# Kernel tuning notes

Measured on AMD Instinct MI355X. Metric: run time of the kernel, lower is better.

The kernel has to match this reference:

```python
import jax, jax.numpy as jnp
import numpy as np

B, HGRID, WGRID = 4, 32, 32
L = 1 + HGRID * WGRID          # cls token + spatial tokens
INPUT_DIM = 512
HEAD_DIM = 512
N_HEAD = 8
QKV_DIM = HEAD_DIM * N_HEAD    # 4096


def pos_embed_2d(h, w, C, dtype):
    """Standard 2D sinusoidal positional embedding, shape (h*w, C)."""
    d = C // 4
    omega = 1.0 / (10000.0 ** (jnp.arange(d, dtype=jnp.float32) / d))
    ey = jnp.arange(h, dtype=jnp.float32)[:, None] * omega      # (h, d)
    ex = jnp.arange(w, dtype=jnp.float32)[:, None] * omega      # (w, d)
    emb_y = jnp.concatenate([jnp.sin(ey), jnp.cos(ey)], -1)     # (h, 2d)
    emb_x = jnp.concatenate([jnp.sin(ex), jnp.cos(ex)], -1)     # (w, 2d)
    emb = jnp.concatenate([
        jnp.broadcast_to(emb_y[:, None, :], (h, w, 2 * d)),
        jnp.broadcast_to(emb_x[None, :, :], (h, w, 2 * d)),
    ], -1)                                                       # (h, w, C)
    return emb.reshape(h * w, C).astype(dtype)


def setup_inputs() -> dict:
    key = jax.random.key(0)
    ks = jax.random.split(key, 16)
    s = 0.02
    inp = {
        "x": jax.random.normal(ks[0], (B, L, INPUT_DIM), dtype=jnp.float32),
        # Q/K/V linear: weight (out, in) as in torch Linear, bias zeros (per _init_bias)
        "Wq": jax.random.normal(ks[1], (QKV_DIM, INPUT_DIM), jnp.float32) * s,
        "bq": jnp.zeros((QKV_DIM,), jnp.float32),
        "Wk": jax.random.normal(ks[2], (QKV_DIM, INPUT_DIM), jnp.float32) * s,
        "bk": jnp.zeros((QKV_DIM,), jnp.float32),
        "Wv": jax.random.normal(ks[3], (QKV_DIM, INPUT_DIM), jnp.float32) * s,
        "bv": jnp.zeros((QKV_DIM,), jnp.float32),
        # 1x1 conv poolers: weight (out_ch, in_ch) = (HEAD_DIM, HEAD_DIM)
        "Wpq": jax.random.normal(ks[4], (HEAD_DIM, HEAD_DIM), jnp.float32) * s,
        "bpq": jax.random.normal(ks[5], (HEAD_DIM,), jnp.float32) * s,
        "Wpk": jax.random.normal(ks[6], (HEAD_DIM, HEAD_DIM), jnp.float32) * s,
        "bpk": jax.random.normal(ks[7], (HEAD_DIM,), jnp.float32) * s,
        "Wpv": jax.random.normal(ks[8], (HEAD_DIM, HEAD_DIM), jnp.float32) * s,
        "bpv": jax.random.normal(ks[9], (HEAD_DIM,), jnp.float32) * s,
        # dispatcher linear: (INPUT_DIM, QKV_DIM)
        "Wd": jax.random.normal(ks[10], (INPUT_DIM, QKV_DIM), jnp.float32) * s,
        "bd": jax.random.normal(ks[11], (INPUT_DIM,), jnp.float32) * s,
        "h": HGRID,
        "w": WGRID,
    }
    return inp


def _pool(t, Wp, bp):
    """AttentionPooler with kernel=1/stride=1: pointwise conv on spatial tokens,
    cls token passed through unchanged. t: (B, n_head, L, head_dim)."""
    cls_tok = t[:, :, :1, :]
    sp = jnp.einsum('bnlc,oc->bnlo', t[:, :, 1:, :], Wp) + bp
    return jnp.concatenate([cls_tok, sp], axis=2)


def reference(x, Wq, bq, Wk, bk, Wv, bv, Wpq, bpq, Wpk, bpk, Wpv, bpv, Wd, bd, h, w):
    Bs, Ls, _ = x.shape

    def proj(Wt, bt):
        y = jnp.einsum('bli,oi->blo', x, Wt) + bt
        return y.reshape(Bs, Ls, N_HEAD, HEAD_DIM).transpose(0, 2, 1, 3)  # (B,nh,L,hd)

    Q = proj(Wq, bq)
    K = proj(Wk, bk)
    V = proj(Wv, bv)

    PQ = _pool(Q, Wpq, bpq)
    PK = _pool(K, Wpk, bpk)
    PV = _pool(V, Wpv, bpv)

    # relative positional encoding added to pooled Q's spatial tokens
    emb = pos_embed_2d(h, w, HEAD_DIM, PQ.dtype)                 # (h*w, hd)
    PQ = jnp.concatenate([PQ[:, :, :1, :], PQ[:, :, 1:, :] + emb], axis=2)

    scale = 1.0 / jnp.sqrt(jnp.asarray(HEAD_DIM, PQ.dtype))
    logits = jnp.einsum('bnqc,bnkc->bnqk', PQ, PK) * scale
    attn = jax.nn.softmax(logits, axis=-1)
    sa = jnp.einsum('bnqk,bnkc->bnqc', attn, PV)

    # skip connection on spatial tokens only (cls row excluded)
    sa = jnp.concatenate([sa[:, :, :1, :], sa[:, :, 1:, :] + Q[:, :, 1:, :]], axis=2)

    stacked = sa.transpose(0, 2, 1, 3).reshape(Bs, Ls, QKV_DIM)
    out = jnp.einsum('blq,oq->blo', stacked, Wd) + bd
    return out
```

## Files before the change

kernel.cpp:

```cpp
#include <hip/hip_runtime.h>


typedef unsigned short u16;
typedef __attribute__((ext_vector_type(8))) short short8;
typedef __attribute__((ext_vector_type(4))) float floatx4;
typedef __attribute__((ext_vector_type(4))) unsigned short us4;

__device__ __forceinline__ u16 f2bf(float f) {
  union { float f; unsigned u; } x; x.f = f;
  unsigned r = (x.u + 0x7fffu + ((x.u >> 16) & 1u)) >> 16;
  return (u16)r;
}
__device__ __forceinline__ float bf2f(u16 u) {
  union { unsigned u; float f; } x; x.u = ((unsigned)u) << 16;
  return x.f;
}

__device__ __forceinline__ void gld_lds16(const void* g, void* l) {
  __builtin_amdgcn_global_load_lds(
      (const __attribute__((address_space(1))) void*)g,
      (__attribute__((address_space(3))) void*)l, 16, 0, 0);
}

struct CvtArgs { const float* src[8]; u16* dst[8]; int n4[8]; };

__global__ __launch_bounds__(256) void cvt_all(CvtArgs a, int total4) {
  int t = blockIdx.x * 256 + threadIdx.x;
  if (t >= total4) return;
#pragma unroll
  for (int s = 0; s < 8; ++s) {
    if (t < a.n4[s]) {
      const float* sp = a.src[s] + (long)t * 4;
      u16* dp = a.dst[s] + (long)t * 4;
      float4 v = *(const float4*)sp;
      dp[0] = f2bf(v.x); dp[1] = f2bf(v.y); dp[2] = f2bf(v.z); dp[3] = f2bf(v.w);
      return;
    }
    t -= a.n4[s];
  }
}

__global__ __launch_bounds__(256) void emb_kernel(float* __restrict__ e) {
  int t = blockIdx.x * 256 + threadIdx.x;
  int c = t & 511, sp = t >> 9;
  int y = sp >> 5, xg = sp & 31;
  int j = c & 127, seg = c >> 7;
  float omega = expf(-(float)j * (9.210340371976184f / 128.f));
  float arg = (float)((seg < 2) ? y : xg) * omega;
  e[t] = (seg & 1) ? cosf(arg) : sinf(arg);
}

__global__ __launch_bounds__(256) void cls_all(
    const u16* __restrict__ Q, const u16* __restrict__ K, const u16* __restrict__ V,
    u16* __restrict__ PQ, u16* __restrict__ PK, u16* __restrict__ PVt) {
  int t = blockIdx.x * 256 + threadIdx.x;
  int bn = t >> 9, c = t & 511;
  long o = (long)bn * 1025 * 512 + c;
  PQ[o] = Q[o];
  PK[o] = K[o];
  PVt[((long)bn * 512 + c) * 1088] = V[o];
}

__global__ __launch_bounds__(256) void softmax_rows(u16* __restrict__ S) {
  int flat = blockIdx.x;
  int xcd = flat & 7, s0 = flat >> 3;
  int zi = s0 / 257, blk = s0 - zi * 257;
  int head = xcd + 8 * zi;
  int wv = threadIdx.x >> 6, lane = threadIdx.x & 63;
  int row_i = blk * 4 + wv;
  if (row_i > 1024) return;
  u16* row = S + ((long)head * 1025 + row_i) * 1088;
  float v[16];
  float mx = -1e30f;
#pragma unroll
  for (int i = 0; i < 4; ++i) {
    us4 p = *(const us4*)(row + i * 256 + lane * 4);
#pragma unroll
    for (int e = 0; e < 4; ++e) { v[i * 4 + e] = bf2f(p[e]); mx = fmaxf(mx, v[i * 4 + e]); }
  }
  float e1024 = (lane == 0) ? bf2f(row[1024]) : -1e30f;
  mx = fmaxf(mx, e1024);
  for (int o = 32; o > 0; o >>= 1) mx = fmaxf(mx, __shfl_xor(mx, o, 64));
  float s = 0.f;
#pragma unroll
  for (int i = 0; i < 16; ++i) { v[i] = __expf(v[i] - mx); s += v[i]; }
  e1024 = (lane == 0) ? __expf(e1024 - mx) : 0.f;
  s += e1024;
  for (int o = 32; o > 0; o >>= 1) s += __shfl_xor(s, o, 64);
  float inv = 1.0f / s;
#pragma unroll
  for (int i = 0; i < 4; ++i) {
    us4 q;
#pragma unroll
    for (int e = 0; e < 4; ++e) q[e] = f2bf(v[i * 4 + e] * inv);
    *(us4*)(row + i * 256 + lane * 4) = q;
  }
  if (lane < 16) {
    us4 q;
#pragma unroll
    for (int e = 0; e < 4; ++e) q[e] = 0;
    if (lane == 0) q[0] = f2bf(e1024 * inv);
    *(us4*)(row + 1024 + lane * 4) = q;
  }
}

__global__ __launch_bounds__(256) void reduce4(const float* __restrict__ part,
                                               const float* __restrict__ bd,
                                               float* __restrict__ out) {
  int t = blockIdx.x * 256 + threadIdx.x;
  long i = (long)t * 4;
  const long STR = 4100ll * 512;
  float4 a = *(const float4*)(part + i);
  float4 b = *(const float4*)(part + i + STR);
  float4 c = *(const float4*)(part + i + 2 * STR);
  float4 d = *(const float4*)(part + i + 3 * STR);
  float4 bb = *(const float4*)(bd + (int)(i & 511));
  float4 r;
  r.x = a.x + b.x + c.x + d.x + bb.x;
  r.y = a.y + b.y + c.y + d.y + bb.y;
  r.z = a.z + b.z + c.z + d.z + bb.z;
  r.w = a.w + b.w + c.w + d.w + bb.w;
  *(float4*)(out + i) = r;
}

struct GP {
  const u16* A; const u16* A2; const u16* B; const u16* B2;
  const float* c0; const float* c1; const float* c2;
  const float* emb; const u16* resid;
  u16* o0; u16* o1; u16* o2;
  float* of; int bz0;
};

template <int MODE>
__global__ __launch_bounds__(256) void gemm_bt(GP g) {
  constexpr int KLEN = (MODE == 5) ? 1024 : ((MODE == 4) ? 1088 : 512);
  constexpr int KITER = KLEN / 64;
  constexpr bool LDSEP = (MODE == 0 || MODE == 1 || MODE == 3 || MODE == 4);
  __shared__ u16 smem[16384];
  u16* As = smem;
  u16* Bs = smem + 8192;
  const int tid = threadIdx.x;
  const int lane = tid & 63;
  const int wv = tid >> 6;
  const int wr = wv >> 1, wc = wv & 1;
  const int ccol = lane & 15;
  const int rgrp = lane >> 4;

  int mt, nt, bz;
  if constexpr (MODE == 3 || MODE == 4) {
    constexpr int PER = (MODE == 3) ? 81 : 36;
    constexpr int NTW = (MODE == 3) ? 9 : 4;
    int flat = blockIdx.x;
    int xcd = flat & 7, s = flat >> 3;
    bz = xcd + 8 * (s / PER);
    int tile = s % PER;
    mt = tile / NTW;
    nt = tile % NTW;
  } else if constexpr (MODE == 1) {
    int flat = blockIdx.x;
    int xcd = flat & 7, s = flat >> 3;
    bz = s >> 7;
    int rem = s & 127;
    mt = xcd * 32 + (rem >> 2);
    nt = rem & 3;
  } else if constexpr (MODE == 2) {
    int flat = blockIdx.x;
    int xcd = flat & 7, s = flat >> 3;
    bz = 0;
    mt = xcd * 32 + (s >> 2);
    nt = s & 3;
  } else {
    mt = blockIdx.y; nt = blockIdx.x; bz = blockIdx.z;
  }
  const int gbz = g.bz0 + bz;

  const u16* Ap = g.A;
  const u16* Bp = g.B;
  if constexpr (MODE == 1) {
    if (bz == 1) { Ap = g.A2; Bp = g.B2; }
  }

  int a_row[4], b_row[4], kx[4];
#pragma unroll
  for (int c = 0; c < 4; ++c) {
    int idx = c * 256 + tid;
    int row = idx >> 3;
    kx[c] = ((idx & 7) ^ (row & 7)) * 8;
    {
      int r = mt * 128 + row;
      int off;
      if constexpr (MODE == 0) { r = r < 4099 ? r : 4099; off = r * 512; }
      else if constexpr (MODE == 1 || MODE == 2) { off = ((r >> 10) * 1025 + 1 + (r & 1023)) * 512; }
      else if constexpr (MODE == 3) { r = r < 1024 ? r : 1024; off = gbz * (1025 * 512) + r * 512; }
      else if constexpr (MODE == 4) { r = r < 1024 ? r : 1024; off = bz * (1025 * 1088) + r * 1088; }
      else { r = r < 4099 ? r : 4099; off = r * 4096; }
      a_row[c] = off;
    }
    {
      int r = nt * 128 + row;
      int off;
      if constexpr (MODE == 3) { r = r < 1024 ? r : 1024; off = gbz * (1025 * 512) + r * 512; }
      else if constexpr (MODE == 4) { off = gbz * (512 * 1088) + r * 1088; }
      else if constexpr (MODE == 5) { off = r * 4096; }
      else { off = r * 512; }
      b_row[c] = off;
    }
  }

  floatx4 acc[4][4];
  {
    float binit[4] = {0.f, 0.f, 0.f, 0.f};
    if constexpr (MODE == 0) {
      int sec = nt >> 5;
      const float* bs = (sec == 0) ? g.c0 : (sec == 1) ? g.c1 : g.c2;
#pragma unroll
      for (int j = 0; j < 4; ++j) binit[j] = bs[(nt & 31) * 128 + wc * 64 + j * 16 + ccol];
    }
    if constexpr (MODE == 1) {
      const float* bs = bz ? g.c1 : g.c0;
#pragma unroll
      for (int j = 0; j < 4; ++j) binit[j] = bs[nt * 128 + wc * 64 + j * 16 + ccol];
    }
    if constexpr (MODE == 2) {
#pragma unroll
      for (int j = 0; j < 4; ++j) binit[j] = g.c0[nt * 128 + wc * 64 + j * 16 + ccol];
    }
#pragma unroll
    for (int i = 0; i < 4; ++i)
#pragma unroll
      for (int j = 0; j < 4; ++j)
#pragma unroll
        for (int rr = 0; rr < 4; ++rr) acc[i][j][rr] = binit[j];
  }

  const int kbase = (MODE == 5) ? bz * 1024 : 0;
  const int l15 = lane & 15;
  const int lq = lane >> 4;
  const int l7 = lane & 7;

  for (int kt = 0; kt < KITER; ++kt) {
    const int k0 = kbase + kt * 64;
#pragma unroll
    for (int c = 0; c < 4; ++c)
      gld_lds16(Ap + a_row[c] + k0 + kx[c], (char*)As + (c * 256 + wv * 64) * 16);
#pragma unroll
    for (int c = 0; c < 4; ++c)
      gld_lds16(Bp + b_row[c] + k0 + kx[c], (char*)Bs + (c * 256 + wv * 64) * 16);
    __syncthreads();
#pragma unroll
    for (int ks = 0; ks < 2; ++ks) {
      const int ch = ((ks * 4 + lq) ^ l7) * 8;
      short8 af[4], bf[4];
#pragma unroll
      for (int i = 0; i < 4; ++i)
        af[i] = *(const short8*)(As + (wr * 64 + i * 16 + l15) * 64 + ch);
#pragma unroll
      for (int j = 0; j < 4; ++j)
        bf[j] = *(const short8*)(Bs + (wc * 64 + j * 16 + l15) * 64 + ch);
#pragma unroll
      for (int i = 0; i < 4; ++i)
#pragma unroll
        for (int j = 0; j < 4; ++j)
          acc[i][j] = __builtin_amdgcn_mfma_f32_16x16x32_bf16(af[i], bf[j], acc[i][j], 0, 0, 0);
    }
    __syncthreads();
  }

  if constexpr (LDSEP) {
#pragma unroll
    for (int i = 0; i < 4; ++i)
#pragma unroll
      for (int j = 0; j < 4; ++j)
#pragma unroll
        for (int rr = 0; rr < 4; ++rr) {
          int lr = wr * 64 + i * 16 + rgrp * 4 + rr;
          int lc = wc * 64 + j * 16 + ccol;
          float v = acc[i][j][rr];
          if constexpr (MODE == 3) v *= 0.04419417382415922f;
          smem[lr * 128 + (lc ^ (rgrp << 4))] = f2bf(v);
        }
    __syncthreads();
#pragma unroll
    for (int q = 0; q < 8; ++q) {
      int cid = q * 256 + tid;
      int r = cid >> 4;
      int c = cid & 15;
      int pc = c ^ ((((unsigned)r >> 2) & 3) << 1);
      short8 val = *(const short8*)(smem + r * 128 + pc * 8);
      int grow = mt * 128 + r;
      if constexpr (MODE == 0) {
        if (grow < 4100) {
          int sec = nt >> 5;
          int col = (nt & 31) * 128 + c * 8;
          u16* ob = (sec == 0) ? g.o0 : (sec == 1) ? g.o1 : g.o2;
          int b = grow / 1025, l = grow - b * 1025;
          int n = col >> 9, ch2 = col & 511;
          *(short8*)(ob + ((long)(b * 8 + n) * 1025 + l) * 512 + ch2) = val;
        }
      } else if constexpr (MODE == 1) {
        int bn = grow >> 10, sp = grow & 1023;
        int gcol = nt * 128 + c * 8;
        short8 outv = val;
        if (bz == 0) {
          const float* ep = g.emb + sp * 512 + gcol;
          float4 e0 = *(const float4*)ep;
          float4 e1 = *(const float4*)(ep + 4);
          float ee[8] = {e0.x, e0.y, e0.z, e0.w, e1.x, e1.y, e1.z, e1.w};
#pragma unroll
          for (int e = 0; e < 8; ++e) outv[e] = (short)f2bf(bf2f((u16)val[e]) + ee[e]);
        }
        u16* dst = (bz == 0) ? g.o0 : g.o1;
        *(short8*)(dst + ((long)bn * 1025 + 1 + sp) * 512 + gcol) = outv;
      } else if constexpr (MODE == 3) {
        if (grow <= 1024) {
          int gcol0 = nt * 128 + c * 8;
          u16* dst = g.o0 + ((long)bz * 1025 + grow) * 1088 + gcol0;
          if (gcol0 + 7 <= 1024) *(short8*)dst = val;
          else if (gcol0 <= 1024) dst[0] = (u16)val[0];
        }
      } else {
        if (grow <= 1024) {
          int gcol0 = nt * 128 + c * 8;
          short8 outv = val;
          if (grow >= 1) {
            short8 rs = *(const short8*)(g.resid + ((long)gbz * 1025 + grow) * 512 + gcol0);
#pragma unroll
            for (int e = 0; e < 8; ++e)
              outv[e] = (short)f2bf(bf2f((u16)val[e]) + bf2f((u16)rs[e]));
          }
          int b = gbz >> 3, n = gbz & 7;
          *(short8*)(g.o0 + (((long)b * 1025 + grow) * 8 + n) * 512 + gcol0) = outv;
        }
      }
    }
  } else {
#pragma unroll
    for (int i = 0; i < 4; ++i) {
#pragma unroll
      for (int j = 0; j < 4; ++j) {
        const int gcol = nt * 128 + wc * 64 + j * 16 + ccol;
#pragma unroll
        for (int rr = 0; rr < 4; ++rr) {
          const int grow = mt * 128 + wr * 64 + i * 16 + rgrp * 4 + rr;
          float v = acc[i][j][rr];
          if constexpr (MODE == 2) {
            int bn = grow >> 10, sp = grow & 1023;
            g.o0[((long)bn * 512 + gcol) * 1088 + 1 + sp] = f2bf(v);
          } else {
            if (grow < 4100)
              g.of[((long)bz * 4100 + grow) * 512 + gcol] = v;
          }
        }
      }
    }
  }
}

extern "C" void kernel_launch(void* const* d_in, const int* in_sizes, int n_in,
                              void* d_out, int out_size, void* d_ws, size_t ws_size,
                              hipStream_t stream) {
  const float* x   = (const float*)d_in[0];
  const float* Wq  = (const float*)d_in[1];
  const float* bq  = (const float*)d_in[2];
  const float* Wk  = (const float*)d_in[3];
  const float* bk  = (const float*)d_in[4];
  const float* Wv  = (const float*)d_in[5];
  const float* bv  = (const float*)d_in[6];
  const float* Wpq = (const float*)d_in[7];
  const float* bpq = (const float*)d_in[8];
  const float* Wpk = (const float*)d_in[9];
  const float* bpk = (const float*)d_in[10];
  const float* Wpv = (const float*)d_in[11];
  const float* bpv = (const float*)d_in[12];
  const float* Wd  = (const float*)d_in[13];
  const float* bd  = (const float*)d_in[14];
  float* out = (float*)d_out;

  char* ws = (char*)d_ws;
  size_t off = 0;
  auto alloc = [&](size_t bytes) {
    char* p = ws + off;
    off += (bytes + 255) & ~(size_t)255;
    return p;
  };
  u16* Wpqb = (u16*)alloc(512ull * 512 * 2);
  u16* Wpkb = (u16*)alloc(512ull * 512 * 2);
  u16* Wpvb = (u16*)alloc(512ull * 512 * 2);
  u16* Wdb  = (u16*)alloc(4096ull * 512 * 2);
  u16* Q    = (u16*)alloc(32ull * 1025 * 512 * 2);
  u16* PQ   = (u16*)alloc(32ull * 1025 * 512 * 2);
  u16* PK   = (u16*)alloc(32ull * 1025 * 512 * 2);
  u16* PVt  = (u16*)alloc(32ull * 512 * 1088 * 2);
  size_t s_off = off;
  u16* K    = (u16*)alloc(32ull * 1025 * 512 * 2);
  u16* V    = (u16*)alloc(32ull * 1025 * 512 * 2);
  u16* xb   = (u16*)alloc(4100ull * 512 * 2);
  u16* Wqb  = (u16*)alloc(4096ull * 512 * 2);
  u16* Wkb  = (u16*)alloc(4096ull * 512 * 2);
  u16* Wvb  = (u16*)alloc(4096ull * 512 * 2);
  float* embp = (float*)alloc(1024ull * 512 * 4);
  size_t fixed_need = off;
  u16* S = (u16*)(ws + s_off);
  float* part = (float*)PQ;
  (void)in_sizes; (void)n_in; (void)out_size;

  const size_t sbytes = 1025ull * 1088 * 2;
  size_t need1 = s_off + 32ull * sbytes;
  size_t need2 = s_off + 16ull * sbytes;
  size_t stk4_off = s_off + ((8ull * sbytes + 255) & ~(size_t)255);
  size_t need4 = stk4_off + 4100ull * 4096 * 2;
  int nchunk;
  u16* stk;
  if (ws_size >= need1)      { nchunk = 1; stk = PK; }
  else if (ws_size >= need2 && ws_size >= fixed_need) { nchunk = 2; stk = PK; }
  else if (ws_size >= need4 && ws_size >= fixed_need) {
    nchunk = 4; stk = (u16*)(ws + stk4_off);
  } else return;
  if (nchunk == 2) {
    size_t stk2_off = s_off + ((16ull * sbytes + 255) & ~(size_t)255);
    if (ws_size >= stk2_off + 4100ull * 4096 * 2) stk = (u16*)(ws + stk2_off);
    else {
      nchunk = 4;
      if (ws_size >= need4) stk = (u16*)(ws + stk4_off);
      else return;
    }
  }
  int hpc = 32 / nchunk;

  CvtArgs ca;
  ca.src[0] = x;   ca.dst[0] = xb;   ca.n4[0] = 4100 * 512 / 4;
  ca.src[1] = Wq;  ca.dst[1] = Wqb;  ca.n4[1] = 4096 * 512 / 4;
  ca.src[2] = Wk;  ca.dst[2] = Wkb;  ca.n4[2] = 4096 * 512 / 4;
  ca.src[3] = Wv;  ca.dst[3] = Wvb;  ca.n4[3] = 4096 * 512 / 4;
  ca.src[4] = Wpq; ca.dst[4] = Wpqb; ca.n4[4] = 512 * 512 / 4;
  ca.src[5] = Wpk; ca.dst[5] = Wpkb; ca.n4[5] = 512 * 512 / 4;
  ca.src[6] = Wpv; ca.dst[6] = Wpvb; ca.n4[6] = 512 * 512 / 4;
  ca.src[7] = Wd;  ca.dst[7] = Wdb;  ca.n4[7] = 512 * 4096 / 4;
  int total4 = 0;
  for (int s = 0; s < 8; ++s) total4 += ca.n4[s];
  cvt_all<<<(total4 + 255) / 256, 256, 0, stream>>>(ca, total4);

  emb_kernel<<<(1024 * 512) / 256, 256, 0, stream>>>(embp);

  {
    GP g = {};
    g.A = xb; g.B = Wqb;
    g.c0 = bq; g.c1 = bk; g.c2 = bv;
    g.o0 = Q; g.o1 = K; g.o2 = V;
    gemm_bt<0><<<dim3(96, 33, 1), 256, 0, stream>>>(g);
  }

  cls_all<<<(32 * 512) / 256, 256, 0, stream>>>(Q, K, V, PQ, PK, PVt);

  {
    GP g = {};
    g.A = Q; g.A2 = K; g.B = Wpqb; g.B2 = Wpkb;
    g.c0 = bpq; g.c1 = bpk; g.emb = embp;
    g.o0 = PQ; g.o1 = PK;
    gemm_bt<1><<<dim3(2048, 1, 1), 256, 0, stream>>>(g);
  }
  {
    GP g = {};
    g.A = V; g.B = Wpvb; g.c0 = bpv; g.o0 = PVt;
    gemm_bt<2><<<dim3(1024, 1, 1), 256, 0, stream>>>(g);
  }

  for (int c = 0; c < nchunk; ++c) {
    GP g3 = {}; g3.A = PQ; g3.B = PK; g3.o0 = S; g3.bz0 = c * hpc;
    gemm_bt<3><<<dim3(81 * hpc, 1, 1), 256, 0, stream>>>(g3);
    softmax_rows<<<257 * hpc, 256, 0, stream>>>(S);
    GP g4 = {}; g4.A = S; g4.B = PVt; g4.resid = Q; g4.o0 = stk; g4.bz0 = c * hpc;
    gemm_bt<4><<<dim3(36 * hpc, 1, 1), 256, 0, stream>>>(g4);
  }

  {
    GP g = {}; g.A = stk; g.B = Wdb; g.of = part;
    gemm_bt<5><<<dim3(4, 33, 4), 256, 0, stream>>>(g);
  }
  reduce4<<<(4100 * 512 / 4 + 255) / 256, 256, 0, stream>>>(part, bd, out);
}
```

Measured before the change: 463.8 us.

## Trim QK^T grid to 8x8 tiles with edge kernel, halve split-K, fuse emb

The QK^T GEMM now covers only the 1024x1024 interior with an 8x8 tile grid instead of 9x9, dropping the mostly-empty edge tiles. A small s_edge kernel computes the last row and column (index 1024) with per-thread dot products. The output GEMM's split-K drops from 4 to 2 partitions, so the reduce kernel reads half as much. The positional-embedding kernel is folded into the conversion kernel to save a launch. Risks include less parallelism in the output GEMM and correctness subtleties in the s_edge handling, for example the s_edge head offset when nh==32.

```diff
diff --git a/kernel.cpp b/kernel.cpp
--- a/kernel.cpp
+++ b/kernel.cpp
@@ -24,9 +24,23 @@
 
 struct CvtArgs { const float* src[8]; u16* dst[8]; int n4[8]; };
 
-__global__ __launch_bounds__(256) void cvt_all(CvtArgs a, int total4) {
+__global__ __launch_bounds__(256) void cvt_all(CvtArgs a, int total4, float* __restrict__ e) {
   int t = blockIdx.x * 256 + threadIdx.x;
-  if (t >= total4) return;
+  if (t >= total4) {
+    int et = (t - total4) * 4;
+    if (et >= 1024 * 512) return;
+#pragma unroll
+    for (int u = 0; u < 4; ++u) {
+      int idx = et + u;
+      int c = idx & 511, sp = idx >> 9;
+      int y = sp >> 5, xg = sp & 31;
+      int j = c & 127, seg = c >> 7;
+      float omega = expf(-(float)j * (9.210340371976184f / 128.f));
+      float arg = (float)((seg < 2) ? y : xg) * omega;
+      e[idx] = (seg & 1) ? cosf(arg) : sinf(arg);
+    }
+    return;
+  }
 #pragma unroll
   for (int s = 0; s < 8; ++s) {
     if (t < a.n4[s]) {
@@ -38,16 +52,6 @@
     }
     t -= a.n4[s];
   }
-}
-
-__global__ __launch_bounds__(256) void emb_kernel(float* __restrict__ e) {
-  int t = blockIdx.x * 256 + threadIdx.x;
-  int c = t & 511, sp = t >> 9;
-  int y = sp >> 5, xg = sp & 31;
-  int j = c & 127, seg = c >> 7;
-  float omega = expf(-(float)j * (9.210340371976184f / 128.f));
-  float arg = (float)((seg < 2) ? y : xg) * omega;
-  e[t] = (seg & 1) ? cosf(arg) : sinf(arg);
 }
 
 __global__ __launch_bounds__(256) void cls_all(
@@ -59,6 +63,44 @@
   PQ[o] = Q[o];
   PK[o] = K[o];
   PVt[((long)bn * 512 + c) * 1088] = V[o];
+}
+
+__global__ __launch_bounds__(256) void s_edge(const u16* __restrict__ PQ,
+                                              const u16* __restrict__ PK,
+                                              u16* __restrict__ S, int nh) {
+  int flat = blockIdx.x;
+  int head, seg;
+  if (nh == 32) {
+    int xcd = flat & 7, s = flat >> 3;
+    head = xcd + 8 * (s >> 2);
+    seg = s & 3;
+  } else {
+    head = flat >> 2;
+    seg = flat & 3;
+  }
+  const u16* pq = PQ + (long)head * 1025 * 512;
+  const u16* pk = PK + (long)head * 1025 * 512;
+  u16* sh = S + (long)head * 1025 * 1088;
+#pragma unroll
+  for (int i = 0; i < 3; ++i) {
+    int local = i * 256 + (int)threadIdx.x;
+    if (local >= 513) continue;
+    int e = seg * 513 + local;
+    if (e >= 2049) continue;
+    int q, kv;
+    if (e < 1025) { q = 1024; kv = e; }
+    else { q = e - 1025; kv = 1024; }
+    const u16* a = pq + (long)q * 512;
+    const u16* b = pk + (long)kv * 512;
+    float acc = 0.f;
+    for (int k8 = 0; k8 < 64; ++k8) {
+      short8 av = *(const short8*)(a + k8 * 8);
+      short8 bv = *(const short8*)(b + k8 * 8);
+#pragma unroll
+      for (int u = 0; u < 8; ++u) acc += bf2f((u16)av[u]) * bf2f((u16)bv[u]);
+    }
+    sh[(long)q * 1088 + kv] = f2bf(acc * 0.04419417382415922f);
+  }
 }
 
 __global__ __launch_bounds__(256) void softmax_rows(u16* __restrict__ S) {
@@ -104,7 +146,7 @@
   }
 }
 
-__global__ __launch_bounds__(256) void reduce4(const float* __restrict__ part,
+__global__ __launch_bounds__(256) void reduce2(const float* __restrict__ part,
                                                const float* __restrict__ bd,
                                                float* __restrict__ out) {
   int t = blockIdx.x * 256 + threadIdx.x;
@@ -112,14 +154,12 @@
   const long STR = 4100ll * 512;
   float4 a = *(const float4*)(part + i);
   float4 b = *(const float4*)(part + i + STR);
-  float4 c = *(const float4*)(part + i + 2 * STR);
-  float4 d = *(const float4*)(part + i + 3 * STR);
   float4 bb = *(const float4*)(bd + (int)(i & 511));
   float4 r;
-  r.x = a.x + b.x + c.x + d.x + bb.x;
-  r.y = a.y + b.y + c.y + d.y + bb.y;
-  r.z = a.z + b.z + c.z + d.z + bb.z;
-  r.w = a.w + b.w + c.w + d.w + bb.w;
+  r.x = a.x + b.x + bb.x;
+  r.y = a.y + b.y + bb.y;
+  r.z = a.z + b.z + bb.z;
+  r.w = a.w + b.w + bb.w;
   *(float4*)(out + i) = r;
 }
 
@@ -133,7 +173,7 @@
 
 template <int MODE>
 __global__ __launch_bounds__(256) void gemm_bt(GP g) {
-  constexpr int KLEN = (MODE == 5) ? 1024 : ((MODE == 4) ? 1088 : 512);
+  constexpr int KLEN = (MODE == 5) ? 2048 : ((MODE == 4) ? 1088 : 512);
   constexpr int KITER = KLEN / 64;
   constexpr bool LDSEP = (MODE == 0 || MODE == 1 || MODE == 3 || MODE == 4);
   __shared__ u16 smem[16384];
@@ -148,8 +188,8 @@
 
   int mt, nt, bz;
   if constexpr (MODE == 3 || MODE == 4) {
-    constexpr int PER = (MODE == 3) ? 81 : 36;
-    constexpr int NTW = (MODE == 3) ? 9 : 4;
+    constexpr int PER = (MODE == 3) ? 64 : 36;
+    constexpr int NTW = (MODE == 3) ? 8 : 4;
     int flat = blockIdx.x;
     int xcd = flat & 7, s = flat >> 3;
     bz = xcd + 8 * (s / PER);
@@ -191,7 +231,7 @@
       int off;
       if constexpr (MODE == 0) { r = r < 4099 ? r : 4099; off = r * 512; }
       else if constexpr (MODE == 1 || MODE == 2) { off = ((r >> 10) * 1025 + 1 + (r & 1023)) * 512; }
-      else if constexpr (MODE == 3) { r = r < 1024 ? r : 1024; off = gbz * (1025 * 512) + r * 512; }
+      else if constexpr (MODE == 3) { off = gbz * (1025 * 512) + r * 512; }
       else if constexpr (MODE == 4) { r = r < 1024 ? r : 1024; off = bz * (1025 * 1088) + r * 1088; }
       else { r = r < 4099 ? r : 4099; off = r * 4096; }
       a_row[c] = off;
@@ -199,7 +239,7 @@
     {
       int r = nt * 128 + row;
       int off;
-      if constexpr (MODE == 3) { r = r < 1024 ? r : 1024; off = gbz * (1025 * 512) + r * 512; }
+      if constexpr (MODE == 3) { off = gbz * (1025 * 512) + r * 512; }
       else if constexpr (MODE == 4) { off = gbz * (512 * 1088) + r * 1088; }
       else if constexpr (MODE == 5) { off = r * 4096; }
       else { off = r * 512; }
@@ -233,7 +273,7 @@
         for (int rr = 0; rr < 4; ++rr) acc[i][j][rr] = binit[j];
   }
 
-  const int kbase = (MODE == 5) ? bz * 1024 : 0;
+  const int kbase = (MODE == 5) ? bz * 2048 : 0;
   const int l15 = lane & 15;
   const int lq = lane >> 4;
   const int l7 = lane & 7;
@@ -312,12 +352,7 @@
         u16* dst = (bz == 0) ? g.o0 : g.o1;
         *(short8*)(dst + ((long)bn * 1025 + 1 + sp) * 512 + gcol) = outv;
       } else if constexpr (MODE == 3) {
-        if (grow <= 1024) {
-          int gcol0 = nt * 128 + c * 8;
-          u16* dst = g.o0 + ((long)bz * 1025 + grow) * 1088 + gcol0;
-          if (gcol0 + 7 <= 1024) *(short8*)dst = val;
-          else if (gcol0 <= 1024) dst[0] = (u16)val[0];
-        }
+        *(short8*)(g.o0 + ((long)bz * 1025 + grow) * 1088 + nt * 128 + c * 8) = val;
       } else {
         if (grow <= 1024) {
           int gcol0 = nt * 128 + c * 8;
@@ -438,9 +473,8 @@
   ca.src[7] = Wd;  ca.dst[7] = Wdb;  ca.n4[7] = 512 * 4096 / 4;
   int total4 = 0;
   for (int s = 0; s < 8; ++s) total4 += ca.n4[s];
-  cvt_all<<<(total4 + 255) / 256, 256, 0, stream>>>(ca, total4);
-
-  emb_kernel<<<(1024 * 512) / 256, 256, 0, stream>>>(embp);
+  int grid1 = (total4 + 1024 * 512 / 4 + 255) / 256;
+  cvt_all<<<grid1, 256, 0, stream>>>(ca, total4, embp);
 
   {
     GP g = {};
@@ -467,7 +501,9 @@
 
   for (int c = 0; c < nchunk; ++c) {
     GP g3 = {}; g3.A = PQ; g3.B = PK; g3.o0 = S; g3.bz0 = c * hpc;
-    gemm_bt<3><<<dim3(81 * hpc, 1, 1), 256, 0, stream>>>(g3);
+    gemm_bt<3><<<dim3(64 * hpc, 1, 1), 256, 0, stream>>>(g3);
+    s_edge<<<hpc * 4, 256, 0, stream>>>(
+        PQ + (long)c * hpc * 1025 * 512, PK + (long)c * hpc * 1025 * 512, S, hpc);
     softmax_rows<<<257 * hpc, 256, 0, stream>>>(S);
     GP g4 = {}; g4.A = S; g4.B = PVt; g4.resid = Q; g4.o0 = stk; g4.bz0 = c * hpc;
     gemm_bt<4><<<dim3(36 * hpc, 1, 1), 256, 0, stream>>>(g4);
@@ -475,7 +511,7 @@
 
   {
     GP g = {}; g.A = stk; g.B = Wdb; g.of = part;
-    gemm_bt<5><<<dim3(4, 33, 4), 256, 0, stream>>>(g);
-  }
-  reduce4<<<(4100 * 512 / 4 + 255) / 256, 256, 0, stream>>>(part, bd, out);
-}
+    gemm_bt<5><<<dim3(4, 33, 2), 256, 0, stream>>>(g);
+  }
+  reduce2<<<(4100 * 512 / 4 + 255) / 256, 256, 0, stream>>>(part, bd, out);
+}
```

Result: no change. 463.9 us (+0.0%).
